# Kernel tuning notes

Hardware: AMD Instinct MI355X
Metric: run time of the kernel (lower is better)

## Reference

```python
import jax, jax.numpy as jnp
import numpy as np

N_NODES = 50000
N_EDGES = 800000
NFEAT = 128
NHID = 64
NLAYER = 3
BN_EPS = 1e-5


def _bn(h, gamma, beta):
    # BatchNorm1d, training-mode batch statistics (biased variance)
    mu = jnp.mean(h, axis=0)
    var = jnp.mean((h - mu) ** 2, axis=0)
    return gamma * (h - mu) * jax.lax.rsqrt(var + BN_EPS) + beta


def setup_inputs() -> dict:
    key = jax.random.key(0)
    ks = jax.random.split(key, 8)
    x = jax.random.normal(ks[0], (N_NODES, NFEAT), dtype=jnp.float32)
    edge_index = jax.random.randint(ks[1], (2, N_EDGES), 0, N_NODES, dtype=jnp.int64)
    # transform: Linear(nfeat, nhid) with bias, then BN
    W_t = jax.random.normal(ks[2], (NFEAT, NHID), dtype=jnp.float32) / np.sqrt(NFEAT)
    b_t = jnp.zeros((NHID,), dtype=jnp.float32)
    g_t = jnp.ones((NHID,), dtype=jnp.float32)
    bb_t = jnp.zeros((NHID,), dtype=jnp.float32)
    # per-layer GIN MLPs (bias=False) and BN affine params, stacked over layers
    W1 = jax.random.normal(ks[3], (NLAYER, NHID, NHID), dtype=jnp.float32) / np.sqrt(NHID)
    W2 = jax.random.normal(ks[4], (NLAYER, NHID, NHID), dtype=jnp.float32) / np.sqrt(NHID)
    gamma = jnp.ones((NLAYER, NHID), dtype=jnp.float32)
    beta = jnp.zeros((NLAYER, NHID), dtype=jnp.float32)
    return {"x": x, "edge_index": edge_index, "W_t": W_t, "b_t": b_t,
            "g_t": g_t, "bb_t": bb_t, "W1": W1, "W2": W2,
            "gamma": gamma, "beta": beta}


def reference(x, edge_index, W_t, b_t, g_t, bb_t, W1, W2, gamma, beta):
    src, dst = edge_index[0], edge_index[1]
    # input transform: Linear + BN
    h = _bn(x @ W_t + b_t, g_t, bb_t)
    for i in range(NLAYER):
        # dropout p=0 -> identity
        # GINConv (eps=0): (1+eps)*h + sum_{j->i} h_j, then 2-layer MLP
        agg = h + jax.ops.segment_sum(h[src], dst, num_segments=N_NODES)
        h = jax.nn.relu(agg @ W1[i]) @ W2[i]
        h = jax.nn.relu(h)
        h = _bn(h, gamma[i], beta[i])
    # per-graph boolean-mask split is a pure partition of rows; return full matrix
    return h
```

## Files before the change

### kernel.cpp

```cpp
#include <hip/hip_runtime.h>

#define NND 50000
#define NED 800000
#define NF  128
#define NH  64
#define BN_EPS 1e-5
#define NCOPY 8
#define SCB  256
#define NSB  ((NND + SCB - 1) / SCB)
#define XNODES (NND / 8)
#define FCH  196

#define WS_HB     0
#define WS_AGG    6400000
#define WS_STATS  12800000
#define WS_DEG    (WS_STATS + 4*NCOPY*128*4)
#define WS_OFFS   (WS_DEG + NND*4)
#define WS_CUR    (WS_OFFS + (NND+4)*4)
#define WS_PARTS  (WS_CUR + NND*4)
#define WS_ESRC   (WS_PARTS + 256*4)

typedef int int4v __attribute__((ext_vector_type(4)));

__device__ __forceinline__ unsigned bfrn(float x) {
    unsigned u = __float_as_uint(x);
    return (u + 0x7fffu + ((u >> 16) & 1u)) >> 16;
}
__device__ __forceinline__ unsigned pk(float lo, float hi) {
    return bfrn(lo) | (bfrn(hi) << 16);
}
__device__ __forceinline__ void upadd(unsigned u, float& lo, float& hi) {
    lo += __uint_as_float(u << 16);
    hi += __uint_as_float(u & 0xffff0000u);
}
__device__ __forceinline__ float ulo(unsigned u) { return __uint_as_float(u << 16); }
__device__ __forceinline__ float uhi(unsigned u) { return __uint_as_float(u & 0xffff0000u); }

__device__ __forceinline__ void bn_derive(const float* __restrict__ st, int c,
                                          const float* __restrict__ g,
                                          const float* __restrict__ b,
                                          float& sc, float& sh) {
    float sum = 0.f, ssq = 0.f;
#pragma unroll
    for (int cp = 0; cp < NCOPY; ++cp) {
        sum += st[cp * 128 + c];
        ssq += st[cp * 128 + 64 + c];
    }
    double mu  = (double)sum / (double)NND;
    double var = (double)ssq / (double)NND - mu * mu;
    if (var < 0.0) var = 0.0;
    double rs = 1.0 / sqrt(var + BN_EPS);
    double scd = (double)g[c] * rs;
    sc = (float)scd;
    sh = (float)((double)b[c] - mu * scd);
}

__global__ __launch_bounds__(256) void k_deg(const int* __restrict__ dst,
                                             int* __restrict__ deg) {
    int xcd = blockIdx.x & 7;
    int chunk = blockIdx.x >> 3;
    int lo = xcd * XNODES;
    const int4v* d4 = (const int4v*)dst;
#pragma unroll
    for (int r = 0; r < 4; ++r) {
        int i = chunk * 1024 + r * 256 + threadIdx.x;
        if (i < NED / 4) {
            int4v d = __builtin_nontemporal_load(d4 + i);
            if ((unsigned)(d.x - lo) < XNODES) atomicAdd(&deg[d.x], 1);
            if ((unsigned)(d.y - lo) < XNODES) atomicAdd(&deg[d.y], 1);
            if ((unsigned)(d.z - lo) < XNODES) atomicAdd(&deg[d.z], 1);
            if ((unsigned)(d.w - lo) < XNODES) atomicAdd(&deg[d.w], 1);
        }
    }
}

__global__ __launch_bounds__(256) void k_fill(const int* __restrict__ src,
                                              const int* __restrict__ dst,
                                              int* __restrict__ cur,
                                              int* __restrict__ esrc) {
    int xcd = blockIdx.x & 7;
    int chunk = blockIdx.x >> 3;
    int lo = xcd * XNODES;
    const int4v* d4 = (const int4v*)dst;
    const int4v* s4 = (const int4v*)src;
#pragma unroll
    for (int r = 0; r < 4; ++r) {
        int i = chunk * 1024 + r * 256 + threadIdx.x;
        if (i < NED / 4) {
            int4v d = __builtin_nontemporal_load(d4 + i);
            int4v s = __builtin_nontemporal_load(s4 + i);
            if ((unsigned)(d.x - lo) < XNODES) esrc[atomicAdd(&cur[d.x], 1)] = s.x;
            if ((unsigned)(d.y - lo) < XNODES) esrc[atomicAdd(&cur[d.y], 1)] = s.y;
            if ((unsigned)(d.z - lo) < XNODES) esrc[atomicAdd(&cur[d.z], 1)] = s.z;
            if ((unsigned)(d.w - lo) < XNODES) esrc[atomicAdd(&cur[d.w], 1)] = s.w;
        }
    }
}

__global__ __launch_bounds__(SCB) void k_part(const int* __restrict__ deg,
                                              int* __restrict__ offs,
                                              int* __restrict__ parts) {
    __shared__ int sd[SCB];
    int t = threadIdx.x;
    int i = blockIdx.x * SCB + t;
    int v = (i < NND) ? deg[i] : 0;
    sd[t] = v;
    __syncthreads();
#pragma unroll
    for (int off = 1; off < SCB; off <<= 1) {
        int u = (t >= off) ? sd[t - off] : 0;
        __syncthreads();
        sd[t] += u;
        __syncthreads();
    }
    if (i < NND) offs[i] = sd[t] - v;
    if (t == SCB - 1) parts[blockIdx.x] = sd[t];
}

__global__ __launch_bounds__(256) void k_scan2(int* __restrict__ parts) {
    __shared__ int sd[256];
    int t = threadIdx.x;
    int v = (t < NSB) ? parts[t] : 0;
    sd[t] = v;
    __syncthreads();
#pragma unroll
    for (int off = 1; off < 256; off <<= 1) {
        int u = (t >= off) ? sd[t - off] : 0;
        __syncthreads();
        sd[t] += u;
        __syncthreads();
    }
    if (t < NSB) parts[t] = sd[t] - v;
}

__global__ __launch_bounds__(256) void k_apply(int* __restrict__ offs,
                                               const int* __restrict__ parts,
                                               int* __restrict__ cur) {
    int i = blockIdx.x * 256 + threadIdx.x;
    if (i < NND) {
        int o = offs[i] + parts[i >> 8];
        offs[i] = o;
        cur[i] = o;
    }
    if (i == NND) offs[NND] = NED;
}

__global__ __launch_bounds__(128) void k_transform(const float* __restrict__ x,
                                                   const float* __restrict__ Wt,
                                                   const float* __restrict__ bt,
                                                   unsigned* __restrict__ hB,
                                                   float* __restrict__ stats) {
    __shared__ __align__(16) unsigned Wlu[NF * NH / 2];
    __shared__ __align__(16) float sT[64 * 68];
    int tid  = threadIdx.x;
    int wave = tid >> 6, lane = tid & 63;
    int ti = lane & 7, tj = lane >> 3;
    int tile = blockIdx.x;
    int base = tile * 64;
    const float4* x4 = (const float4*)x;

#pragma unroll
    for (int r = 0; r < 16; ++r) {
        int i4 = r * 128 + tid;
        float4 w = ((const float4*)Wt)[i4];
        uint2 wp; wp.x = pk(w.x, w.y); wp.y = pk(w.z, w.w);
        ((uint2*)Wlu)[i4] = wp;
    }

    float acc[8][4];
#pragma unroll
    for (int i = 0; i < 8; ++i)
#pragma unroll
        for (int j = 0; j < 4; ++j) acc[i][j] = 0.f;

    int cw = wave * 32 + tj * 4;

    for (int ch = 0; ch < 2; ++ch) {
        __syncthreads();
        float4 pf[8];
#pragma unroll
        for (int s = 0; s < 8; ++s) {
            int flat = s * 128 + tid;
            int nl = flat >> 4, q = flat & 15;
            pf[s] = make_float4(0.f, 0.f, 0.f, 0.f);
            if (base + nl < NND) pf[s] = x4[(size_t)(base + nl) * 32 + ch * 16 + q];
        }
#pragma unroll
        for (int s = 0; s < 8; ++s) {
            int flat = s * 128 + tid;
            int nl = flat >> 4, q = flat & 15;
            sT[(q * 4 + 0) * 68 + nl] = pf[s].x;
            sT[(q * 4 + 1) * 68 + nl] = pf[s].y;
            sT[(q * 4 + 2) * 68 + nl] = pf[s].z;
            sT[(q * 4 + 3) * 68 + nl] = pf[s].w;
        }
        __syncthreads();
#pragma unroll 4
        for (int k = 0; k < 64; ++k) {
            const float* ap = &sT[k * 68 + ti * 8];
            float4 alo = *(const float4*)ap;
            float4 ahi = *(const float4*)(ap + 4);
            uint2 wu = *(const uint2*)&Wlu[(ch * 64 + k) * 32 + (cw >> 1)];
            float a8[8] = {alo.x, alo.y, alo.z, alo.w, ahi.x, ahi.y, ahi.z, ahi.w};
            float w4[4] = {ulo(wu.x), uhi(wu.x), ulo(wu.y), uhi(wu.y)};
#pragma unroll
            for (int i = 0; i < 8; ++i)
#pragma unroll
                for (int j = 0; j < 4; ++j) acc[i][j] += a8[i] * w4[j];
        }
    }

    float4 bv = *(const float4*)&bt[cw];
    float bj[4] = {bv.x, bv.y, bv.z, bv.w};

    float s4[4] = {0.f, 0.f, 0.f, 0.f}, q4[4] = {0.f, 0.f, 0.f, 0.f};
    uint2* hB2 = (uint2*)hB;
#pragma unroll
    for (int i = 0; i < 8; ++i) {
        int n = base + ti * 8 + i;
        if (n < NND) {
            float o[4];
#pragma unroll
            for (int j = 0; j < 4; ++j) {
                o[j] = acc[i][j] + bj[j];
                s4[j] += o[j];
                q4[j] += o[j] * o[j];
            }
            uint2 ov; ov.x = pk(o[0], o[1]); ov.y = pk(o[2], o[3]);
            hB2[(size_t)n * 16 + wave * 8 + tj] = ov;
        }
    }
#pragma unroll
    for (int m = 1; m < 8; m <<= 1) {
#pragma unroll
        for (int j = 0; j < 4; ++j) {
            s4[j] += __shfl_xor(s4[j], m);
            q4[j] += __shfl_xor(q4[j], m);
        }
    }
    if (ti == 0) {
        int slot = (tile & (NCOPY - 1)) * 128;
#pragma unroll
        for (int j = 0; j < 4; ++j) {
            atomicAdd(&stats[slot + cw + j], s4[j]);
            atomicAdd(&stats[slot + 64 + cw + j], q4[j]);
        }
    }
}

__global__ __launch_bounds__(256) void k_agg(const uint4* __restrict__ hB4,
                                             uint4* __restrict__ aggB4,
                                             const float* __restrict__ stats,
                                             const float* __restrict__ g,
                                             const float* __restrict__ b,
                                             const int* __restrict__ offs,
                                             const int* __restrict__ esrc) {
    int tid  = threadIdx.x;
    int lane = tid & 63;
    int wv   = tid >> 6;
    int n = blockIdx.x * 4 + wv;
    int q = lane & 7;
    int r = lane >> 3;

    float scl, shl;
    bn_derive(stats, lane, g, b, scl, shl);

    int e0 = offs[n], e1 = offs[n + 1];
    int deg = e1 - e0;

    float a[8];
#pragma unroll
    for (int i = 0; i < 8; ++i) a[i] = 0.f;

    if (r == 0) {
        uint4 u = hB4[(size_t)n * 8 + q];
        upadd(u.x, a[0], a[1]); upadd(u.y, a[2], a[3]);
        upadd(u.z, a[4], a[5]); upadd(u.w, a[6], a[7]);
    }

    for (int bb = e0; bb < e1; bb += 64) {
        int m = e1 - bb; if (m > 64) m = 64;
        int idx = (lane < m) ? esrc[bb + lane] : 0;
        int t = 0;
        for (; t + 32 <= m; t += 32) {
            int j0 = __shfl(idx, t + r);
            int j1 = __shfl(idx, t + 8 + r);
            int j2 = __shfl(idx, t + 16 + r);
            int j3 = __shfl(idx, t + 24 + r);
            uint4 u0 = hB4[(size_t)j0 * 8 + q];
            uint4 u1 = hB4[(size_t)j1 * 8 + q];
            uint4 u2 = hB4[(size_t)j2 * 8 + q];
            uint4 u3 = hB4[(size_t)j3 * 8 + q];
            upadd(u0.x, a[0], a[1]); upadd(u0.y, a[2], a[3]);
            upadd(u0.z, a[4], a[5]); upadd(u0.w, a[6], a[7]);
            upadd(u1.x, a[0], a[1]); upadd(u1.y, a[2], a[3]);
            upadd(u1.z, a[4], a[5]); upadd(u1.w, a[6], a[7]);
            upadd(u2.x, a[0], a[1]); upadd(u2.y, a[2], a[3]);
            upadd(u2.z, a[4], a[5]); upadd(u2.w, a[6], a[7]);
            upadd(u3.x, a[0], a[1]); upadd(u3.y, a[2], a[3]);
            upadd(u3.z, a[4], a[5]); upadd(u3.w, a[6], a[7]);
        }
        for (; t < m; t += 8) {
            int e = t + r;
            int j = __shfl(idx, e & 63);
            if (e < m) {
                uint4 u = hB4[(size_t)j * 8 + q];
                upadd(u.x, a[0], a[1]); upadd(u.y, a[2], a[3]);
                upadd(u.z, a[4], a[5]); upadd(u.w, a[6], a[7]);
            }
        }
    }

#pragma unroll
    for (int msk = 8; msk <= 32; msk <<= 1)
#pragma unroll
        for (int i = 0; i < 8; ++i) a[i] += __shfl_xor(a[i], msk);

    float sc8[8], sh8[8];
#pragma unroll
    for (int j = 0; j < 8; ++j) {
        sc8[j] = __shfl(scl, q * 8 + j);
        sh8[j] = __shfl(shl, q * 8 + j);
    }

    if (r == 0) {
        float dn = (float)(deg + 1);
        float o[8];
#pragma unroll
        for (int j = 0; j < 8; ++j) o[j] = sc8[j] * a[j] + dn * sh8[j];
        uint4 ov;
        ov.x = pk(o[0], o[1]); ov.y = pk(o[2], o[3]);
        ov.z = pk(o[4], o[5]); ov.w = pk(o[6], o[7]);
        aggB4[(size_t)n * 8 + q] = ov;
    }
}

__global__ __launch_bounds__(128) void k_mlp(const uint4* __restrict__ aggB4,
                                             float* __restrict__ outF,
                                             unsigned* __restrict__ hBo,
                                             float* __restrict__ stats,
                                             const float* __restrict__ W1,
                                             const float* __restrict__ W2) {
    __shared__ __align__(16) float W1l[NH * NH];
    __shared__ __align__(16) float W2l[NH * NH];
    __shared__ __align__(16) float sT[64 * 68];
    int tid  = threadIdx.x;
    int wave = tid >> 6, lane = tid & 63;
    int ti = lane & 7, tj = lane >> 3;
    int tile = blockIdx.x;
    int base = tile * 64;
    int cw = wave * 32 + tj * 4;

#pragma unroll
    for (int r = 0; r < 8; ++r) {
        int i4 = r * 128 + tid;
        ((float4*)W1l)[i4] = ((const float4*)W1)[i4];
        ((float4*)W2l)[i4] = ((const float4*)W2)[i4];
    }
#pragma unroll
    for (int s = 0; s < 4; ++s) {
        int i4 = s * 128 + tid;
        int nl = i4 >> 3, q = i4 & 7;
        uint4 u = make_uint4(0u, 0u, 0u, 0u);
        if (base + nl < NND) u = aggB4[(size_t)(base + nl) * 8 + q];
        sT[(q * 8 + 0) * 68 + nl] = ulo(u.x);
        sT[(q * 8 + 1) * 68 + nl] = uhi(u.x);
        sT[(q * 8 + 2) * 68 + nl] = ulo(u.y);
        sT[(q * 8 + 3) * 68 + nl] = uhi(u.y);
        sT[(q * 8 + 4) * 68 + nl] = ulo(u.z);
        sT[(q * 8 + 5) * 68 + nl] = uhi(u.z);
        sT[(q * 8 + 6) * 68 + nl] = ulo(u.w);
        sT[(q * 8 + 7) * 68 + nl] = uhi(u.w);
    }
    __syncthreads();

    float a1[8][4];
#pragma unroll
    for (int i = 0; i < 8; ++i)
#pragma unroll
        for (int j = 0; j < 4; ++j) a1[i][j] = 0.f;
#pragma unroll 4
    for (int k = 0; k < 64; ++k) {
        const float* ap = &sT[k * 68 + ti * 8];
        float4 alo = *(const float4*)ap;
        float4 ahi = *(const float4*)(ap + 4);
        float4 wv  = *(const float4*)&W1l[k * NH + cw];
        float a8[8] = {alo.x, alo.y, alo.z, alo.w, ahi.x, ahi.y, ahi.z, ahi.w};
        float w4[4] = {wv.x, wv.y, wv.z, wv.w};
#pragma unroll
        for (int i = 0; i < 8; ++i)
#pragma unroll
            for (int j = 0; j < 4; ++j) a1[i][j] += a8[i] * w4[j];
    }
#pragma unroll
    for (int i = 0; i < 8; ++i)
#pragma unroll
        for (int j = 0; j < 4; ++j) a1[i][j] = fmaxf(a1[i][j], 0.f);

    __syncthreads();
#pragma unroll
    for (int j = 0; j < 4; ++j) {
        float* p = &sT[(cw + j) * 68 + ti * 8];
        float4 lo = {a1[0][j], a1[1][j], a1[2][j], a1[3][j]};
        float4 hi = {a1[4][j], a1[5][j], a1[6][j], a1[7][j]};
        *(float4*)p = lo;
        *(float4*)(p + 4) = hi;
    }
    __syncthreads();

    float a2[8][4];
#pragma unroll
    for (int i = 0; i < 8; ++i)
#pragma unroll
        for (int j = 0; j < 4; ++j) a2[i][j] = 0.f;
#pragma unroll 4
    for (int k = 0; k < 64; ++k) {
        const float* ap = &sT[k * 68 + ti * 8];
        float4 alo = *(const float4*)ap;
        float4 ahi = *(const float4*)(ap + 4);
        float4 wv  = *(const float4*)&W2l[k * NH + cw];
        float a8[8] = {alo.x, alo.y, alo.z, alo.w, ahi.x, ahi.y, ahi.z, ahi.w};
        float w4[4] = {wv.x, wv.y, wv.z, wv.w};
#pragma unroll
        for (int i = 0; i < 8; ++i)
#pragma unroll
            for (int j = 0; j < 4; ++j) a2[i][j] += a8[i] * w4[j];
    }

    float s4[4] = {0.f, 0.f, 0.f, 0.f}, q4[4] = {0.f, 0.f, 0.f, 0.f};
    uint2* hBo2 = (uint2*)hBo;
#pragma unroll
    for (int i = 0; i < 8; ++i) {
        int n = base + ti * 8 + i;
        if (n < NND) {
            float o[4];
#pragma unroll
            for (int j = 0; j < 4; ++j) {
                o[j] = fmaxf(a2[i][j], 0.f);
                s4[j] += o[j];
                q4[j] += o[j] * o[j];
            }
            if (outF) *(float4*)&outF[(size_t)n * NH + cw] = *(float4*)&o[0];
            if (hBo) {
                uint2 ov; ov.x = pk(o[0], o[1]); ov.y = pk(o[2], o[3]);
                hBo2[(size_t)n * 16 + wave * 8 + tj] = ov;
            }
        }
    }
#pragma unroll
    for (int m = 1; m < 8; m <<= 1) {
#pragma unroll
        for (int j = 0; j < 4; ++j) {
            s4[j] += __shfl_xor(s4[j], m);
            q4[j] += __shfl_xor(q4[j], m);
        }
    }
    if (ti == 0) {
        int slot = (tile & (NCOPY - 1)) * 128;
#pragma unroll
        for (int j = 0; j < 4; ++j) {
            atomicAdd(&stats[slot + cw + j], s4[j]);
            atomicAdd(&stats[slot + 64 + cw + j], q4[j]);
        }
    }
}

__global__ __launch_bounds__(256) void k_bnout(float* __restrict__ h,
                                               const float* __restrict__ stats,
                                               const float* __restrict__ g,
                                               const float* __restrict__ b) {
    __shared__ float sl[128];
    int tid = threadIdx.x;
    if (tid < 64) {
        float sc, sh;
        bn_derive(stats, tid, g, b, sc, sh);
        sl[tid]      = sc;
        sl[64 + tid] = sh;
    }
    __syncthreads();
    int i4 = blockIdx.x * 256 + tid;
    if (i4 < NND * NH / 4) {
        int cg = i4 & 15;
        float4 v   = ((float4*)h)[i4];
        float4 scv = *(float4*)&sl[cg * 4];
        float4 shv = *(float4*)&sl[64 + cg * 4];
        v.x = v.x * scv.x + shv.x;
        v.y = v.y * scv.y + shv.y;
        v.z = v.z * scv.z + shv.z;
        v.w = v.w * scv.w + shv.w;
        ((float4*)h)[i4] = v;
    }
}

extern "C" void kernel_launch(void* const* d_in, const int* in_sizes, int n_in,
                              void* d_out, int out_size, void* d_ws, size_t ws_size,
                              hipStream_t stream) {
    const float* x     = (const float*)d_in[0];
    const int*   ei    = (const int*)d_in[1];
    const float* Wt    = (const float*)d_in[2];
    const float* bt    = (const float*)d_in[3];
    const float* gt    = (const float*)d_in[4];
    const float* bbt   = (const float*)d_in[5];
    const float* W1    = (const float*)d_in[6];
    const float* W2    = (const float*)d_in[7];
    const float* gamma = (const float*)d_in[8];
    const float* beta  = (const float*)d_in[9];
    float* out = (float*)d_out;

    char* ws = (char*)d_ws;
    unsigned* hB    = (unsigned*)(ws + WS_HB);
    unsigned* aggB  = (unsigned*)(ws + WS_AGG);
    float*    stats = (float*)(ws + WS_STATS);
    int*      deg   = (int*)(ws + WS_DEG);
    int*      offs  = (int*)(ws + WS_OFFS);
    int*      cur   = (int*)(ws + WS_CUR);
    int*      parts = (int*)(ws + WS_PARTS);
    int*      esrc  = (int*)(ws + WS_ESRC);

    float* st0 = stats;
    float* st1 = stats + NCOPY * 128;
    float* st2 = stats + 2 * NCOPY * 128;
    float* st3 = stats + 3 * NCOPY * 128;

    const int* srcv = ei;
    const int* dstv = ei + NED;

    hipMemsetAsync(stats, 0, 4 * NCOPY * 128 * 4 + NND * 4, stream);

    const int PGRID = FCH * 8;
    k_deg<<<PGRID, 256, 0, stream>>>(dstv, deg);
    k_part<<<NSB, SCB, 0, stream>>>(deg, offs, parts);
    k_scan2<<<1, 256, 0, stream>>>(parts);
    k_apply<<<NSB, 256, 0, stream>>>(offs, parts, cur);
    k_fill<<<PGRID, 256, 0, stream>>>(srcv, dstv, cur, esrc);

    const int NT = 782;
    const int NB = NND / 4;

    k_transform<<<NT, 128, 0, stream>>>(x, Wt, bt, hB, st0);

    k_agg<<<NB, 256, 0, stream>>>((const uint4*)hB, (uint4*)aggB, st0, gt, bbt, offs, esrc);
    k_mlp<<<NT, 128, 0, stream>>>((const uint4*)aggB, nullptr, hB, st1, W1, W2);

    k_agg<<<NB, 256, 0, stream>>>((const uint4*)hB, (uint4*)aggB, st1, gamma, beta, offs, esrc);
    k_mlp<<<NT, 128, 0, stream>>>((const uint4*)aggB, nullptr, hB, st2, W1 + 4096, W2 + 4096);

    k_agg<<<NB, 256, 0, stream>>>((const uint4*)hB, (uint4*)aggB, st2, gamma + 64, beta + 64, offs, esrc);
    k_mlp<<<NT, 128, 0, stream>>>((const uint4*)aggB, out, nullptr, st3, W1 + 8192, W2 + 8192);

    k_bnout<<<(NND * NH / 4 + 255) / 256, 256, 0, stream>>>(out, st3, gamma + 128, beta + 128);
}
```

Measured before the change: 323.3 us.

## Fuse degree counting and input transform into one horizontally-fused kernel launch

Merges the degree-histogram kernel and the input Linear transform into a single launch, with block ranges split by blockIdx so the two independent jobs can run concurrently and one launch is saved. The transform blocks grow to 256 threads so every thread helps load tiles, but only the first 128 do the FMA work. Nontemporal loads on the edge arrays are also replaced with plain int4 loads. In exchange, half of each transform block idles during compute, and the shared-memory allocation now also applies to degree blocks, which may lower their occupancy.

```diff
diff --git a/kernel.cpp b/kernel.cpp
--- a/kernel.cpp
+++ b/kernel.cpp
@@ -10,6 +10,8 @@
 #define NSB  ((NND + SCB - 1) / SCB)
 #define XNODES (NND / 8)
 #define FCH  196
+#define NT   782
+#define PGRID (FCH * 8)
 
 #define WS_HB     0
 #define WS_AGG    6400000
@@ -20,8 +22,6 @@
 #define WS_PARTS  (WS_CUR + NND*4)
 #define WS_ESRC   (WS_PARTS + 256*4)
 
-typedef int int4v __attribute__((ext_vector_type(4)));
-
 __device__ __forceinline__ unsigned bfrn(float x) {
     unsigned u = __float_as_uint(x);
     return (u + 0x7fffu + ((u >> 16) & 1u)) >> 16;
@@ -55,21 +55,131 @@
     sh = (float)((double)b[c] - mu * scd);
 }
 
-__global__ __launch_bounds__(256) void k_deg(const int* __restrict__ dst,
-                                             int* __restrict__ deg) {
-    int xcd = blockIdx.x & 7;
-    int chunk = blockIdx.x >> 3;
-    int lo = xcd * XNODES;
-    const int4v* d4 = (const int4v*)dst;
-#pragma unroll
-    for (int r = 0; r < 4; ++r) {
-        int i = chunk * 1024 + r * 256 + threadIdx.x;
-        if (i < NED / 4) {
-            int4v d = __builtin_nontemporal_load(d4 + i);
-            if ((unsigned)(d.x - lo) < XNODES) atomicAdd(&deg[d.x], 1);
-            if ((unsigned)(d.y - lo) < XNODES) atomicAdd(&deg[d.y], 1);
-            if ((unsigned)(d.z - lo) < XNODES) atomicAdd(&deg[d.z], 1);
-            if ((unsigned)(d.w - lo) < XNODES) atomicAdd(&deg[d.w], 1);
+__global__ __launch_bounds__(256) void k_dtf(const int* __restrict__ dst,
+                                             int* __restrict__ deg,
+                                             const float* __restrict__ x,
+                                             const float* __restrict__ Wt,
+                                             const float* __restrict__ bt,
+                                             unsigned* __restrict__ hB,
+                                             float* __restrict__ stats) {
+    __shared__ __align__(16) unsigned Wlu[NF * NH / 2];
+    __shared__ __align__(16) float sT[64 * 68];
+    int tid = threadIdx.x;
+
+    if (blockIdx.x >= NT) {
+        int dbid = blockIdx.x - NT;
+        int xcd = dbid & 7;
+        int chunk = dbid >> 3;
+        int lo = xcd * XNODES;
+        const int4* d4 = (const int4*)dst;
+#pragma unroll
+        for (int r = 0; r < 4; ++r) {
+            int i = chunk * 1024 + r * 256 + tid;
+            if (i < NED / 4) {
+                int4 d = d4[i];
+                if ((unsigned)(d.x - lo) < XNODES) atomicAdd(&deg[d.x], 1);
+                if ((unsigned)(d.y - lo) < XNODES) atomicAdd(&deg[d.y], 1);
+                if ((unsigned)(d.z - lo) < XNODES) atomicAdd(&deg[d.z], 1);
+                if ((unsigned)(d.w - lo) < XNODES) atomicAdd(&deg[d.w], 1);
+            }
+        }
+        return;
+    }
+
+    int tile = blockIdx.x;
+    int base = tile * 64;
+    const float4* x4 = (const float4*)x;
+
+#pragma unroll
+    for (int r = 0; r < 8; ++r) {
+        int i4 = r * 256 + tid;
+        float4 w = ((const float4*)Wt)[i4];
+        uint2 wp; wp.x = pk(w.x, w.y); wp.y = pk(w.z, w.w);
+        ((uint2*)Wlu)[i4] = wp;
+    }
+
+    int wave = tid >> 6, lane = tid & 63;
+    int ti = lane & 7, tj = lane >> 3;
+    int cw = wave * 32 + tj * 4;
+
+    float acc[8][4];
+#pragma unroll
+    for (int i = 0; i < 8; ++i)
+#pragma unroll
+        for (int j = 0; j < 4; ++j) acc[i][j] = 0.f;
+
+    for (int ch = 0; ch < 2; ++ch) {
+        __syncthreads();
+        float4 pf[4];
+#pragma unroll
+        for (int s = 0; s < 4; ++s) {
+            int flat = s * 256 + tid;
+            int nl = flat >> 4, q = flat & 15;
+            pf[s] = make_float4(0.f, 0.f, 0.f, 0.f);
+            if (base + nl < NND) pf[s] = x4[(size_t)(base + nl) * 32 + ch * 16 + q];
+        }
+#pragma unroll
+        for (int s = 0; s < 4; ++s) {
+            int flat = s * 256 + tid;
+            int nl = flat >> 4, q = flat & 15;
+            sT[(q * 4 + 0) * 68 + nl] = pf[s].x;
+            sT[(q * 4 + 1) * 68 + nl] = pf[s].y;
+            sT[(q * 4 + 2) * 68 + nl] = pf[s].z;
+            sT[(q * 4 + 3) * 68 + nl] = pf[s].w;
+        }
+        __syncthreads();
+        if (tid < 128) {
+#pragma unroll 4
+            for (int k = 0; k < 64; ++k) {
+                const float* ap = &sT[k * 68 + ti * 8];
+                float4 alo = *(const float4*)ap;
+                float4 ahi = *(const float4*)(ap + 4);
+                uint2 wu = *(const uint2*)&Wlu[(ch * 64 + k) * 32 + (cw >> 1)];
+                float a8[8] = {alo.x, alo.y, alo.z, alo.w, ahi.x, ahi.y, ahi.z, ahi.w};
+                float w4[4] = {ulo(wu.x), uhi(wu.x), ulo(wu.y), uhi(wu.y)};
+#pragma unroll
+                for (int i = 0; i < 8; ++i)
+#pragma unroll
+                    for (int j = 0; j < 4; ++j) acc[i][j] += a8[i] * w4[j];
+            }
+        }
+    }
+    if (tid >= 128) return;
+
+    float4 bv = *(const float4*)&bt[cw];
+    float bj[4] = {bv.x, bv.y, bv.z, bv.w};
+
+    float s4[4] = {0.f, 0.f, 0.f, 0.f}, q4[4] = {0.f, 0.f, 0.f, 0.f};
+    uint2* hB2 = (uint2*)hB;
+#pragma unroll
+    for (int i = 0; i < 8; ++i) {
+        int n = base + ti * 8 + i;
+        if (n < NND) {
+            float o[4];
+#pragma unroll
+            for (int j = 0; j < 4; ++j) {
+                o[j] = acc[i][j] + bj[j];
+                s4[j] += o[j];
+                q4[j] += o[j] * o[j];
+            }
+            uint2 ov; ov.x = pk(o[0], o[1]); ov.y = pk(o[2], o[3]);
+            hB2[(size_t)n * 16 + wave * 8 + tj] = ov;
+        }
+    }
+#pragma unroll
+    for (int m = 1; m < 8; m <<= 1) {
+#pragma unroll
+        for (int j = 0; j < 4; ++j) {
+            s4[j] += __shfl_xor(s4[j], m);
+            q4[j] += __shfl_xor(q4[j], m);
+        }
+    }
+    if (ti == 0) {
+        int slot = (tile & (NCOPY - 1)) * 128;
+#pragma unroll
+        for (int j = 0; j < 4; ++j) {
+            atomicAdd(&stats[slot + cw + j], s4[j]);
+            atomicAdd(&stats[slot + 64 + cw + j], q4[j]);
         }
     }
 }
@@ -81,14 +191,14 @@
     int xcd = blockIdx.x & 7;
     int chunk = blockIdx.x >> 3;
     int lo = xcd * XNODES;
-    const int4v* d4 = (const int4v*)dst;
-    const int4v* s4 = (const int4v*)src;
+    const int4* d4 = (const int4*)dst;
+    const int4* s4 = (const int4*)src;
 #pragma unroll
     for (int r = 0; r < 4; ++r) {
         int i = chunk * 1024 + r * 256 + threadIdx.x;
         if (i < NED / 4) {
-            int4v d = __builtin_nontemporal_load(d4 + i);
-            int4v s = __builtin_nontemporal_load(s4 + i);
+            int4 d = d4[i];
+            int4 s = s4[i];
             if ((unsigned)(d.x - lo) < XNODES) esrc[atomicAdd(&cur[d.x], 1)] = s.x;
             if ((unsigned)(d.y - lo) < XNODES) esrc[atomicAdd(&cur[d.y], 1)] = s.y;
             if ((unsigned)(d.z - lo) < XNODES) esrc[atomicAdd(&cur[d.z], 1)] = s.z;
@@ -143,109 +253,6 @@
         cur[i] = o;
     }
     if (i == NND) offs[NND] = NED;
-}
-
-__global__ __launch_bounds__(128) void k_transform(const float* __restrict__ x,
-                                                   const float* __restrict__ Wt,
-                                                   const float* __restrict__ bt,
-                                                   unsigned* __restrict__ hB,
-                                                   float* __restrict__ stats) {
-    __shared__ __align__(16) unsigned Wlu[NF * NH / 2];
-    __shared__ __align__(16) float sT[64 * 68];
-    int tid  = threadIdx.x;
-    int wave = tid >> 6, lane = tid & 63;
-    int ti = lane & 7, tj = lane >> 3;
-    int tile = blockIdx.x;
-    int base = tile * 64;
-    const float4* x4 = (const float4*)x;
-
-#pragma unroll
-    for (int r = 0; r < 16; ++r) {
-        int i4 = r * 128 + tid;
-        float4 w = ((const float4*)Wt)[i4];
-        uint2 wp; wp.x = pk(w.x, w.y); wp.y = pk(w.z, w.w);
-        ((uint2*)Wlu)[i4] = wp;
-    }
-
-    float acc[8][4];
-#pragma unroll
-    for (int i = 0; i < 8; ++i)
-#pragma unroll
-        for (int j = 0; j < 4; ++j) acc[i][j] = 0.f;
-
-    int cw = wave * 32 + tj * 4;
-
-    for (int ch = 0; ch < 2; ++ch) {
-        __syncthreads();
-        float4 pf[8];
-#pragma unroll
-        for (int s = 0; s < 8; ++s) {
-            int flat = s * 128 + tid;
-            int nl = flat >> 4, q = flat & 15;
-            pf[s] = make_float4(0.f, 0.f, 0.f, 0.f);
-            if (base + nl < NND) pf[s] = x4[(size_t)(base + nl) * 32 + ch * 16 + q];
-        }
-#pragma unroll
-        for (int s = 0; s < 8; ++s) {
-            int flat = s * 128 + tid;
-            int nl = flat >> 4, q = flat & 15;
-            sT[(q * 4 + 0) * 68 + nl] = pf[s].x;
-            sT[(q * 4 + 1) * 68 + nl] = pf[s].y;
-            sT[(q * 4 + 2) * 68 + nl] = pf[s].z;
-            sT[(q * 4 + 3) * 68 + nl] = pf[s].w;
-        }
-        __syncthreads();
-#pragma unroll 4
-        for (int k = 0; k < 64; ++k) {
-            const float* ap = &sT[k * 68 + ti * 8];
-            float4 alo = *(const float4*)ap;
-            float4 ahi = *(const float4*)(ap + 4);
-            uint2 wu = *(const uint2*)&Wlu[(ch * 64 + k) * 32 + (cw >> 1)];
-            float a8[8] = {alo.x, alo.y, alo.z, alo.w, ahi.x, ahi.y, ahi.z, ahi.w};
-            float w4[4] = {ulo(wu.x), uhi(wu.x), ulo(wu.y), uhi(wu.y)};
-#pragma unroll
-            for (int i = 0; i < 8; ++i)
-#pragma unroll
-                for (int j = 0; j < 4; ++j) acc[i][j] += a8[i] * w4[j];
-        }
-    }
-
-    float4 bv = *(const float4*)&bt[cw];
-    float bj[4] = {bv.x, bv.y, bv.z, bv.w};
-
-    float s4[4] = {0.f, 0.f, 0.f, 0.f}, q4[4] = {0.f, 0.f, 0.f, 0.f};
-    uint2* hB2 = (uint2*)hB;
-#pragma unroll
-    for (int i = 0; i < 8; ++i) {
-        int n = base + ti * 8 + i;
-        if (n < NND) {
-            float o[4];
-#pragma unroll
-            for (int j = 0; j < 4; ++j) {
-                o[j] = acc[i][j] + bj[j];
-                s4[j] += o[j];
-                q4[j] += o[j] * o[j];
-            }
-            uint2 ov; ov.x = pk(o[0], o[1]); ov.y = pk(o[2], o[3]);
-            hB2[(size_t)n * 16 + wave * 8 + tj] = ov;
-        }
-    }
-#pragma unroll
-    for (int m = 1; m < 8; m <<= 1) {
-#pragma unroll
-        for (int j = 0; j < 4; ++j) {
-            s4[j] += __shfl_xor(s4[j], m);
-            q4[j] += __shfl_xor(q4[j], m);
-        }
-    }
-    if (ti == 0) {
-        int slot = (tile & (NCOPY - 1)) * 128;
-#pragma unroll
-        for (int j = 0; j < 4; ++j) {
-            atomicAdd(&stats[slot + cw + j], s4[j]);
-            atomicAdd(&stats[slot + 64 + cw + j], q4[j]);
-        }
-    }
 }
 
 __global__ __launch_bounds__(256) void k_agg(const uint4* __restrict__ hB4,
@@ -527,17 +534,13 @@
 
     hipMemsetAsync(stats, 0, 4 * NCOPY * 128 * 4 + NND * 4, stream);
 
-    const int PGRID = FCH * 8;
-    k_deg<<<PGRID, 256, 0, stream>>>(dstv, deg);
+    k_dtf<<<NT + PGRID, 256, 0, stream>>>(dstv, deg, x, Wt, bt, hB, st0);
     k_part<<<NSB, SCB, 0, stream>>>(deg, offs, parts);
     k_scan2<<<1, 256, 0, stream>>>(parts);
     k_apply<<<NSB, 256, 0, stream>>>(offs, parts, cur);
     k_fill<<<PGRID, 256, 0, stream>>>(srcv, dstv, cur, esrc);
 
-    const int NT = 782;
     const int NB = NND / 4;
-
-    k_transform<<<NT, 128, 0, stream>>>(x, Wt, bt, hB, st0);
 
     k_agg<<<NB, 256, 0, stream>>>((const uint4*)hB, (uint4*)aggB, st0, gt, bbt, offs, esrc);
     k_mlp<<<NT, 128, 0, stream>>>((const uint4*)aggB, nullptr, hB, st1, W1, W2);
```

Result: faster. 301.2 us (-6.9%).
